# Kernel tuning notes

Measured on AMD Instinct MI355X. Metric: run time of the kernel, lower is better.

## Reference

```python
import jax, jax.numpy as jnp
from jax import lax
import numpy as np

B, N, C, T = 64, 25, 128, 256
EPS = 1e-5


def setup_inputs() -> dict:
    key = jax.random.key(0)
    ks = jax.random.split(key, 4)
    x = jax.random.normal(ks[0], (B, N, C, T), dtype=jnp.float32)
    adj = jax.random.uniform(ks[1], (N, N), dtype=jnp.float32)
    # row-normalize adjacency like a typical GCN propagation matrix
    adj = adj / jnp.sum(adj, axis=1, keepdims=True)
    # xavier-uniform-ish linear weight [out, in]
    lim = float(np.sqrt(6.0 / (C + C)))
    W_gcn = jax.random.uniform(ks[2], (C, C), minval=-lim, maxval=lim, dtype=jnp.float32)
    b_gcn = jnp.zeros((C,), jnp.float32)
    W_conv = jax.random.normal(ks[3], (C, C, 3), dtype=jnp.float32) * (1.0 / np.sqrt(3 * C))
    b_conv = jnp.zeros((C,), jnp.float32)
    return dict(
        x=x, adj=adj, W_gcn=W_gcn, b_gcn=b_gcn, W_conv=W_conv, b_conv=b_conv,
        tc_gamma=jnp.ones((C,), jnp.float32), tc_beta=jnp.zeros((C,), jnp.float32),
        tc_mean=jnp.zeros((C,), jnp.float32), tc_var=jnp.ones((C,), jnp.float32),
        bn_gamma=jnp.ones((C,), jnp.float32), bn_beta=jnp.zeros((C,), jnp.float32),
        bn_mean=jnp.zeros((C,), jnp.float32), bn_var=jnp.ones((C,), jnp.float32),
    )


def _bn(x, gamma, beta, mean, var, axis):
    # eval-mode batchnorm over channel `axis`
    shape = [1] * x.ndim
    shape[axis] = -1
    g = gamma.reshape(shape)
    b = beta.reshape(shape)
    m = mean.reshape(shape)
    v = var.reshape(shape)
    return g * (x - m) * lax.rsqrt(v + EPS) + b


def reference(x, adj, W_gcn, b_gcn, W_conv, b_conv,
              tc_gamma, tc_beta, tc_mean, tc_var,
              bn_gamma, bn_beta, bn_mean, bn_var):
    # x: [B, N, C, T]; in_channels == out_channels so residual is identity
    b_, n_, c_, t_ = x.shape
    residual = x
    # spatial GCN for all timesteps at once: linear over feature dim, then adj matmul over nodes
    h = jnp.einsum('bnct,oc->bnot', x, W_gcn) + b_gcn[None, None, :, None]
    h = jnp.einsum('mn,bnot->bmot', adj, h)  # [B, N, C, T]
    # temporal conv1d over T for every (batch, node) pair at once
    hc = h.reshape(b_ * n_, c_, t_)
    y = lax.conv_general_dilated(hc, W_conv, window_strides=(1,), padding=[(1, 1)],
                                 dimension_numbers=('NCH', 'OIH', 'NCH'))
    y = y + b_conv[None, :, None]
    y = _bn(y, tc_gamma, tc_beta, tc_mean, tc_var, axis=1)
    y = jax.nn.relu(y)
    y = y.reshape(b_, n_, c_, t_)
    # residual add, block batchnorm over channels, relu
    y = y + residual
    y = _bn(y, bn_gamma, bn_beta, bn_mean, bn_var, axis=2)
    y = jax.nn.relu(y)
    return y
```

## Files before the change

### kernel.cpp

```cpp
#include <hip/hip_runtime.h>
#include <hip/hip_bf16.h>
#include <stdint.h>

#define Bn 64
#define Nn 25
#define Cn 128
#define Tn 256
#define EPSC 1e-5f

typedef short bf16x8 __attribute__((ext_vector_type(8)));
typedef float f32x4 __attribute__((ext_vector_type(4)));
typedef int   i32x4 __attribute__((ext_vector_type(4)));

static constexpr size_t X2T_BYTES  = (size_t)Bn * Nn * Tn * Cn * 2;
static constexpr size_t WEFF_OFF   = X2T_BYTES;
static constexpr size_t WEFF_BYTES = (size_t)3 * 128 * 128 * 2;
static constexpr size_t EPI_OFF    = WEFF_OFF + WEFF_BYTES;
static constexpr size_t ROWSUM_OFF = EPI_OFF + (size_t)7 * 128 * 4;
static constexpr size_t ZPAGE_OFF  = ROWSUM_OFF + 256;
static constexpr size_t WS_NEEDED  = ZPAGE_OFF + 256;

__device__ __forceinline__ uint16_t f2bf(float f) {
    uint32_t u = __builtin_bit_cast(uint32_t, f);
    u = (u + 0x7FFFu + ((u >> 16) & 1u)) >> 16;
    return (uint16_t)u;
}

__device__ __forceinline__ void dma16(const void* gsrc, void* ldst) {
    __builtin_amdgcn_global_load_lds(
        (const __attribute__((address_space(1))) unsigned int*)gsrc,
        (__attribute__((address_space(3))) unsigned int*)ldst, 16, 0, 0);
}

__global__ __launch_bounds__(128) void prep_kernel(
    const float* __restrict__ adj, const float* __restrict__ Wg,
    const float* __restrict__ bg,  const float* __restrict__ Wc,
    const float* __restrict__ bc,
    const float* __restrict__ tg,  const float* __restrict__ tb_,
    const float* __restrict__ tm,  const float* __restrict__ tv,
    const float* __restrict__ bng, const float* __restrict__ bnb,
    const float* __restrict__ bnm, const float* __restrict__ bnv,
    uint16_t* __restrict__ weff, float* __restrict__ epi, float* __restrict__ rowsum,
    uint32_t* __restrict__ zpage)
{
    int blk = blockIdx.x;
    int tid = threadIdx.x;
    if (blk < 384) {
        int k = blk >> 7, o = blk & 127;
        float acc = 0.f;
        for (int i = 0; i < 128; ++i) {
            float wc = Wc[(o * 128 + i) * 3 + k];
            acc = fmaf(wc, Wg[i * 128 + tid], acc);
        }
        weff[((size_t)(k * 128 + o)) * 128 + tid] = f2bf(acc);
    } else {
        int o = tid;
        float b0 = 0.f, b1 = 0.f, b2 = 0.f;
        for (int i = 0; i < 128; ++i) {
            float g = bg[i];
            b0 = fmaf(Wc[(o * 128 + i) * 3 + 0], g, b0);
            b1 = fmaf(Wc[(o * 128 + i) * 3 + 1], g, b1);
            b2 = fmaf(Wc[(o * 128 + i) * 3 + 2], g, b2);
        }
        float a1  = tg[o] * rsqrtf(tv[o] + EPSC);
        float c1p = tb_[o] - a1 * tm[o] + a1 * bc[o];
        float a2  = bng[o] * rsqrtf(bnv[o] + EPSC);
        float c2  = bnb[o] - a2 * bnm[o];
        epi[0 * 128 + o] = a1;
        epi[1 * 128 + o] = c1p;
        epi[2 * 128 + o] = a2;
        epi[3 * 128 + o] = c2;
        epi[4 * 128 + o] = a1 * b0;
        epi[5 * 128 + o] = a1 * b1;
        epi[6 * 128 + o] = a1 * b2;
        if (tid < Nn) {
            float s = 0.f;
            for (int n = 0; n < Nn; ++n) s += adj[tid * Nn + n];
            rowsum[tid] = s;
        }
        if (tid < 64) zpage[tid] = 0u;
    }
}

__global__ __launch_bounds__(256) void adjmix_kernel(
    const float* __restrict__ x, const float* __restrict__ adj,
    uint16_t* __restrict__ x2t)
{
    __shared__ float adjs[Nn * Nn];
    __shared__ float tr[2][32][33];

    int bid = blockIdx.x;
    int b  = bid >> 5;
    int rem = bid & 31;
    int cb = rem >> 3, tb = rem & 7;
    int c0 = cb * 32, t0 = tb * 32;
    int tid = threadIdx.x;

    for (int i = tid; i < Nn * Nn; i += 256) adjs[i] = adj[i];
    __syncthreads();

    int cl = tid >> 3;
    int t4 = (tid & 7) * 4;

    float acc[Nn][4];
#pragma unroll
    for (int m = 0; m < Nn; ++m)
#pragma unroll
        for (int j = 0; j < 4; ++j) acc[m][j] = 0.f;

    for (int n = 0; n < Nn; ++n) {
        const float4 v = *reinterpret_cast<const float4*>(
            x + (((size_t)(b * Nn + n) * Cn + c0 + cl) * Tn + t0 + t4));
#pragma unroll
        for (int m = 0; m < Nn; ++m) {
            float a = adjs[m * Nn + n];
            acc[m][0] = fmaf(a, v.x, acc[m][0]);
            acc[m][1] = fmaf(a, v.y, acc[m][1]);
            acc[m][2] = fmaf(a, v.z, acc[m][2]);
            acc[m][3] = fmaf(a, v.w, acc[m][3]);
        }
    }

    int c2   = tid & 15;
    int trow0 = tid >> 4;

#pragma unroll
    for (int m = 0; m < Nn; ++m) {
        int mb = m & 1;
        tr[mb][cl][t4 + 0] = acc[m][0];
        tr[mb][cl][t4 + 1] = acc[m][1];
        tr[mb][cl][t4 + 2] = acc[m][2];
        tr[mb][cl][t4 + 3] = acc[m][3];
        __syncthreads();
#pragma unroll
        for (int p = 0; p < 2; ++p) {
            int trow = trow0 + p * 16;
            uint32_t h0 = f2bf(tr[mb][c2 * 2 + 0][trow]);
            uint32_t h1 = f2bf(tr[mb][c2 * 2 + 1][trow]);
            uint32_t u = h0 | (h1 << 16);
            size_t elem = ((size_t)(b * Nn + m) * Tn + (t0 + trow)) * Cn + c0 + c2 * 2;
            *reinterpret_cast<uint32_t*>(x2t + elem) = u;
        }
    }
}

__global__ __launch_bounds__(256, 2) void conv_kernel(
    const uint16_t* __restrict__ x2t, const uint16_t* __restrict__ weff,
    const float* __restrict__ x, const float* __restrict__ epi,
    const float* __restrict__ rowsum, const char* __restrict__ zpage,
    float* __restrict__ out)
{
    constexpr int ROWB = 256;
    constexpr int BUFB = 34 * ROWB;
    __shared__ uint16_t lds[2 * 34 * 128];
    char* ldsb = (char*)lds;

    int bid = blockIdx.x;
    int m   = bid % Nn;

    int tid = threadIdx.x;
    int w  = tid >> 6;
    int l  = tid & 63;
    int lo = l & 15;
    int hi = l >> 4;
    int o0 = w * 32;

    const char*  xp2 = (const char*)x2t + (size_t)bid * Tn * Cn * 2;
    const short* wp  = (const short*)weff;

    bf16x8 bw[3][4][2];
#pragma unroll
    for (int kk = 0; kk < 3; ++kk)
#pragma unroll
        for (int cc = 0; cc < 4; ++cc)
#pragma unroll
            for (int f = 0; f < 2; ++f) {
                int o = o0 + f * 16 + lo;
                bw[kk][cc][f] = *reinterpret_cast<const bf16x8*>(
                    wp + ((size_t)(kk * 128 + o)) * 128 + cc * 32 + hi * 8);
            }

    float a1[2], c1[2], a2[2], c2v[2], g0[2], g1[2], g2[2];
#pragma unroll
    for (int f = 0; f < 2; ++f) {
        int o = o0 + f * 16 + lo;
        a1[f]  = epi[0 * 128 + o];
        c1[f]  = epi[1 * 128 + o];
        a2[f]  = epi[2 * 128 + o];
        c2v[f] = epi[3 * 128 + o];
        g0[f]  = epi[4 * 128 + o];
        g1[f]  = epi[5 * 128 + o];
        g2[f]  = epi[6 * 128 + o];
    }
    float rs = rowsum[m];
    const size_t obase = (size_t)bid * Cn;

    auto stage = [&](int it, int bufByte) {
        int t0 = it * 32;
#pragma unroll
        for (int oi = 0; oi < 2; ++oi) {
            int op = w + oi * 4;
            int rowbase = op * 4;
            int r  = rowbase + (l >> 4);
            int cg = l & 15;
            int gt = t0 - 1 + r;
            int sc = cg ^ (r & 7);
            const char* src = (gt >= 0 && gt < Tn)
                ? xp2 + ((size_t)gt * Cn + sc * 8) * 2
                : zpage + sc * 16;
            dma16(src, ldsb + bufByte + rowbase * ROWB);
        }
        if (w == 0 && l < 32) {
            int rowbase = 32;
            int r  = rowbase + (l >> 4);
            int cg = l & 15;
            int gt = t0 - 1 + r;
            int sc = cg ^ (r & 7);
            const char* src = (gt >= 0 && gt < Tn)
                ? xp2 + ((size_t)gt * Cn + sc * 8) * 2
                : zpage + sc * 16;
            dma16(src, ldsb + bufByte + rowbase * ROWB);
        }
    };

    int cur = 0;
    stage(0, 0);
    asm volatile("s_waitcnt vmcnt(0)" ::: "memory");
    __syncthreads();

    for (int it = 0; it < 8; ++it) {
        int nxt = cur ^ 1;
        if (it < 7) stage(it + 1, nxt * BUFB);

        int tq = it * 32;

        f32x4 r4[2][2];
        size_t idx4[2][2];
#pragma unroll
        for (int j = 0; j < 2; ++j)
#pragma unroll
            for (int f = 0; f < 2; ++f) {
                int o   = o0 + f * 16 + lo;
                int tb4 = tq + j * 16 + hi * 4;
                idx4[j][f] = (obase + o) * Tn + tb4;
                r4[j][f] = *reinterpret_cast<const f32x4*>(x + idx4[j][f]);
            }

        f32x4 acc[2][2];
#pragma unroll
        for (int j = 0; j < 2; ++j)
#pragma unroll
            for (int f = 0; f < 2; ++f) acc[j][f] = (f32x4){0.f, 0.f, 0.f, 0.f};

#pragma unroll
        for (int kk = 0; kk < 3; ++kk)
#pragma unroll
            for (int cc = 0; cc < 4; ++cc) {
                bf16x8 af[2];
#pragma unroll
                for (int j = 0; j < 2; ++j) {
                    int lrow  = j * 16 + lo + kk;
                    int lbyte = cur * BUFB + lrow * ROWB +
                                ((cc * 64 + hi * 16) ^ ((lrow & 7) << 4));
                    af[j] = *reinterpret_cast<const bf16x8*>(ldsb + lbyte);
                }
#pragma unroll
                for (int j = 0; j < 2; ++j)
#pragma unroll
                    for (int f = 0; f < 2; ++f)
                        acc[j][f] = __builtin_amdgcn_mfma_f32_16x16x32_bf16(
                            af[j], bw[kk][cc][f], acc[j][f], 0, 0, 0);
            }

#pragma unroll
        for (int j = 0; j < 2; ++j)
#pragma unroll
            for (int f = 0; f < 2; ++f) {
                int tb4 = tq + j * 16 + hi * 4;
                f32x4 ov;
#pragma unroll
                for (int qq = 0; qq < 4; ++qq) {
                    int t = tb4 + qq;
                    float gbv = g1[f];
                    if (t > 0)      gbv += g0[f];
                    if (t < Tn - 1) gbv += g2[f];
                    float z = fmaxf(fmaf(a1[f], acc[j][f][qq], fmaf(rs, gbv, c1[f])), 0.f);
                    ov[qq] = fmaxf(fmaf(a2[f], z + r4[j][f][qq], c2v[f]), 0.f);
                }
                *reinterpret_cast<f32x4*>(out + idx4[j][f]) = ov;
            }

        asm volatile("s_waitcnt vmcnt(0)" ::: "memory");
        __syncthreads();
        cur = nxt;
    }
}

extern "C" void kernel_launch(void* const* d_in, const int* in_sizes, int n_in,
                              void* d_out, int out_size, void* d_ws, size_t ws_size,
                              hipStream_t stream) {
    const float* x    = (const float*)d_in[0];
    const float* adj  = (const float*)d_in[1];
    const float* Wg   = (const float*)d_in[2];
    const float* bg   = (const float*)d_in[3];
    const float* Wc   = (const float*)d_in[4];
    const float* bc   = (const float*)d_in[5];
    const float* tg   = (const float*)d_in[6];
    const float* tb_  = (const float*)d_in[7];
    const float* tm   = (const float*)d_in[8];
    const float* tv   = (const float*)d_in[9];
    const float* bng  = (const float*)d_in[10];
    const float* bnb  = (const float*)d_in[11];
    const float* bnm  = (const float*)d_in[12];
    const float* bnv  = (const float*)d_in[13];

    if (ws_size < WS_NEEDED) return;

    char* ws = (char*)d_ws;
    uint16_t* x2t    = (uint16_t*)ws;
    uint16_t* weff   = (uint16_t*)(ws + WEFF_OFF);
    float*    epi    = (float*)(ws + EPI_OFF);
    float*    rowsum = (float*)(ws + ROWSUM_OFF);
    char*     zpage  = ws + ZPAGE_OFF;
    float*    out    = (float*)d_out;

    prep_kernel<<<385, 128, 0, stream>>>(adj, Wg, bg, Wc, bc, tg, tb_, tm, tv,
                                         bng, bnb, bnm, bnv, weff, epi, rowsum,
                                         (uint32_t*)zpage);
    adjmix_kernel<<<2048, 256, 0, stream>>>(x, adj, x2t);
    conv_kernel<<<Bn * Nn, 256, 0, stream>>>(x2t, weff, x, epi, rowsum, zpage, out);
}
```

Baseline: 213.1 us.

## Split conv over time halves, widen adjmix stores, raise conv occupancy

```diff
diff --git a/kernel.cpp b/kernel.cpp
--- a/kernel.cpp
+++ b/kernel.cpp
@@ -87,7 +87,7 @@
     uint16_t* __restrict__ x2t)
 {
     __shared__ float adjs[Nn * Nn];
-    __shared__ float tr[2][32][33];
+    __shared__ float tr[2][2][32][33];
 
     int bid = blockIdx.x;
     int b  = bid >> 5;
@@ -121,30 +121,38 @@
         }
     }
 
-    int c2   = tid & 15;
-    int trow0 = tid >> 4;
-
-#pragma unroll
-    for (int m = 0; m < Nn; ++m) {
-        int mb = m & 1;
-        tr[mb][cl][t4 + 0] = acc[m][0];
-        tr[mb][cl][t4 + 1] = acc[m][1];
-        tr[mb][cl][t4 + 2] = acc[m][2];
-        tr[mb][cl][t4 + 3] = acc[m][3];
+    int h    = tid & 127;
+    int half = tid >> 7;
+    int trow = h >> 2;
+    int cq   = h & 3;
+
+#pragma unroll
+    for (int p = 0; p < 13; ++p) {
+        int m0  = 2 * p;
+        int buf = p & 1;
+#pragma unroll
+        for (int j = 0; j < 4; ++j) tr[buf][0][cl][t4 + j] = acc[m0][j];
+        if (m0 + 1 < Nn) {
+#pragma unroll
+            for (int j = 0; j < 4; ++j) tr[buf][1][cl][t4 + j] = acc[m0 + 1][j];
+        }
         __syncthreads();
-#pragma unroll
-        for (int p = 0; p < 2; ++p) {
-            int trow = trow0 + p * 16;
-            uint32_t h0 = f2bf(tr[mb][c2 * 2 + 0][trow]);
-            uint32_t h1 = f2bf(tr[mb][c2 * 2 + 1][trow]);
-            uint32_t u = h0 | (h1 << 16);
-            size_t elem = ((size_t)(b * Nn + m) * Tn + (t0 + trow)) * Cn + c0 + c2 * 2;
-            *reinterpret_cast<uint32_t*>(x2t + elem) = u;
-        }
-    }
-}
-
-__global__ __launch_bounds__(256, 2) void conv_kernel(
+        int mm = m0 + half;
+        if (mm < Nn) {
+            i32x4 u;
+#pragma unroll
+            for (int k2 = 0; k2 < 4; ++k2) {
+                uint32_t lo16 = f2bf(tr[buf][half][cq * 8 + 2 * k2 + 0][trow]);
+                uint32_t hi16 = f2bf(tr[buf][half][cq * 8 + 2 * k2 + 1][trow]);
+                u[k2] = (int)(lo16 | (hi16 << 16));
+            }
+            size_t elem = ((size_t)(b * Nn + mm) * Tn + (t0 + trow)) * Cn + c0 + cq * 8;
+            *reinterpret_cast<i32x4*>(x2t + elem) = u;
+        }
+    }
+}
+
+__global__ __launch_bounds__(256, 4) void conv_kernel(
     const uint16_t* __restrict__ x2t, const uint16_t* __restrict__ weff,
     const float* __restrict__ x, const float* __restrict__ epi,
     const float* __restrict__ rowsum, const char* __restrict__ zpage,
@@ -156,7 +164,10 @@
     char* ldsb = (char*)lds;
 
     int bid = blockIdx.x;
-    int m   = bid % Nn;
+    int bm  = bid >> 1;
+    int th  = bid & 1;
+    int m   = bm % Nn;
+    int T0  = th * 128;
 
     int tid = threadIdx.x;
     int w  = tid >> 6;
@@ -165,7 +176,7 @@
     int hi = l >> 4;
     int o0 = w * 32;
 
-    const char*  xp2 = (const char*)x2t + (size_t)bid * Tn * Cn * 2;
+    const char*  xp2 = (const char*)x2t + (size_t)bm * Tn * Cn * 2;
     const short* wp  = (const short*)weff;
 
     bf16x8 bw[3][4][2];
@@ -193,10 +204,10 @@
         g2[f]  = epi[6 * 128 + o];
     }
     float rs = rowsum[m];
-    const size_t obase = (size_t)bid * Cn;
+    const size_t obase = (size_t)bm * Cn;
 
     auto stage = [&](int it, int bufByte) {
-        int t0 = it * 32;
+        int t0 = T0 + it * 32;
 #pragma unroll
         for (int oi = 0; oi < 2; ++oi) {
             int op = w + oi * 4;
@@ -228,11 +239,11 @@
     asm volatile("s_waitcnt vmcnt(0)" ::: "memory");
     __syncthreads();
 
-    for (int it = 0; it < 8; ++it) {
+    for (int it = 0; it < 4; ++it) {
         int nxt = cur ^ 1;
-        if (it < 7) stage(it + 1, nxt * BUFB);
-
-        int tq = it * 32;
+        if (it < 3) stage(it + 1, nxt * BUFB);
+
+        int tq = T0 + it * 32;
 
         f32x4 r4[2][2];
         size_t idx4[2][2];
@@ -328,5 +339,5 @@
                                          bng, bnb, bnm, bnv, weff, epi, rowsum,
                                          (uint32_t*)zpage);
     adjmix_kernel<<<2048, 256, 0, stream>>>(x, adj, x2t);
-    conv_kernel<<<Bn * Nn, 256, 0, stream>>>(x2t, weff, x, epi, rowsum, zpage, out);
-}
+    conv_kernel<<<Bn * Nn * 2, 256, 0, stream>>>(x2t, weff, x, epi, rowsum, zpage, out);
+}
```

After: 446.8 us. 2.1x slower.
